# Optimization experiments

Hardware: AMD Instinct MI355X
Metric: run time of the kernel (lower is better)

Reference implementation:

```python
import jax, jax.numpy as jnp
import numpy as np

N = 100_000   # nodes
E = 1_600_000 # directed edges
G = 2048      # graphs in batch
NF = 78       # input node features
DIM = 32      # GIN hidden dim
L = 5         # num GIN layers
OUT = 128     # output_dim
BN_EPS = 1e-5


def setup_inputs() -> dict:
    key = jax.random.key(0)
    ks = jax.random.split(key, 8)
    s = 0.1
    return {
        "x": jax.random.normal(ks[0], (N, NF), jnp.float32),
        "edge_index": jax.random.randint(ks[1], (2, E), 0, N, jnp.int32),
        "batch": jnp.sort(jax.random.randint(ks[2], (N,), 0, G, jnp.int32)),
        "W1_0": (jax.random.normal(ks[3], (NF, DIM), jnp.float32) * s),
        "W1_rest": (jax.random.normal(ks[4], (L - 1, DIM, DIM), jnp.float32) * s),
        "b1": jnp.zeros((L, DIM), jnp.float32),
        "W2": (jax.random.normal(ks[5], (L, DIM, DIM), jnp.float32) * s),
        "b2": jnp.zeros((L, DIM), jnp.float32),
        "gamma": jnp.ones((L, DIM), jnp.float32),
        "beta": jnp.zeros((L, DIM), jnp.float32),
        "Wfc": (jax.random.normal(ks[6], (DIM, OUT), jnp.float32) * s),
        "bfc": jnp.zeros((OUT,), jnp.float32),
    }


def reference(x, edge_index, batch, W1_0, W1_rest, b1, W2, b2, gamma, beta, Wfc, bfc):
    src, dst = edge_index[0], edge_index[1]
    h = x
    for i in range(L):
        # GINConv (eps=0): h_i' = MLP(h_i + sum_{j->i} h_j)
        agg = jax.ops.segment_sum(h[src], dst, num_segments=N)  # [N, d]
        h = h + agg
        W1 = W1_0 if i == 0 else W1_rest[i - 1]
        h = jnp.maximum(h @ W1 + b1[i], 0.0) @ W2[i] + b2[i]
        # ReLU then BatchNorm1d (training mode: batch stats, biased var)
        h = jnp.maximum(h, 0.0)
        mu = h.mean(axis=0)
        var = h.var(axis=0)
        h = gamma[i] * (h - mu) * jax.lax.rsqrt(var + BN_EPS) + beta[i]
    pooled = jax.ops.segment_sum(h, batch, num_segments=G)  # global_add_pool [G, DIM]
    return jnp.maximum(pooled @ Wfc + bfc, 0.0)  # dropout is identity (eval)
```

## Files before the change

### kernel.cpp

```cpp
#include <hip/hip_runtime.h>
#include <hip/hip_fp16.h>

#define N_NODES 100000
#define N_EDGES 1600000
#define N_GRAPHS 2048
#define NFEAT 78
#define DIM 32
#define NLAYERS 5
#define OUTD 128
#define BN_EPS 1e-5f
#define NPB 32
#define NBUK 391
#define BNODES 256
#define STRIDE 4608
#define EPB 4096
#define NSLOTS2 ((N_NODES / NPB + 63) / 64)

__device__ __forceinline__ float2 up2(unsigned u) {
    __half2 h = *reinterpret_cast<__half2*>(&u);
    return __half22float2(h);
}
__device__ __forceinline__ unsigned pk2(float a, float b) {
    __half2 h = __floats2half2_rn(a, b);
    return *reinterpret_cast<unsigned*>(&h);
}

__global__ __launch_bounds__(256) void bfill2_kernel(
    const int* __restrict__ ei, int* __restrict__ bcnt, int* __restrict__ bdata)
{
    __shared__ int cur[NBUK];
    __shared__ int gbl[NBUK];
    int tid = threadIdx.x;
    int base = blockIdx.x * EPB;

    for (int i = tid; i < NBUK; i += 256) cur[i] = 0;
    __syncthreads();

    int ew[16];
    int eb[16];
    const int4* s4 = (const int4*)ei;
    const int4* d4 = (const int4*)(ei + N_EDGES);
#pragma unroll
    for (int c = 0; c < 4; ++c) {
        int eidx = base + c * 1024 + tid * 4;
        if (eidx < N_EDGES) {
            int4 sv = s4[eidx >> 2];
            int4 dv = d4[eidx >> 2];
            ew[c*4+0] = sv.x | ((dv.x & 255) << 17); eb[c*4+0] = dv.x >> 8;
            ew[c*4+1] = sv.y | ((dv.y & 255) << 17); eb[c*4+1] = dv.y >> 8;
            ew[c*4+2] = sv.z | ((dv.z & 255) << 17); eb[c*4+2] = dv.z >> 8;
            ew[c*4+3] = sv.w | ((dv.w & 255) << 17); eb[c*4+3] = dv.w >> 8;
        } else {
            eb[c*4+0] = eb[c*4+1] = eb[c*4+2] = eb[c*4+3] = -1;
            ew[c*4+0] = ew[c*4+1] = ew[c*4+2] = ew[c*4+3] = 0;
        }
    }

    int slot[16];
#pragma unroll
    for (int k = 0; k < 16; ++k)
        slot[k] = (eb[k] >= 0) ? atomicAdd(&cur[eb[k]], 1) : 0;
    __syncthreads();

    for (int b = tid; b < NBUK; b += 256) {
        int c = cur[b];
        gbl[b] = (c > 0) ? atomicAdd(&bcnt[b], c) : 0;
    }
    __syncthreads();

#pragma unroll
    for (int k = 0; k < 16; ++k) {
        int b = eb[k];
        if (b >= 0) {
            int pos = gbl[b] + slot[k];
            if (pos < STRIDE) bdata[b * STRIDE + pos] = ew[k];
        }
    }
}

__global__ __launch_bounds__(512) void bscan_kernel(
    const int* __restrict__ bcnt, int* __restrict__ bbase)
{
    __shared__ int sd[512];
    int t = threadIdx.x;
    int v = (t < NBUK) ? min(bcnt[t], STRIDE) : 0;
    sd[t] = v; __syncthreads();
    for (int off = 1; off < 512; off <<= 1) {
        int a = (t >= off) ? sd[t - off] : 0;
        __syncthreads();
        sd[t] += a;
        __syncthreads();
    }
    if (t < NBUK) bbase[t + 1] = sd[t];
    if (t == 0) bbase[0] = 0;
}

__global__ __launch_bounds__(256) void cfill2_kernel(
    const int* __restrict__ bcnt, const int* __restrict__ bbase,
    const int* __restrict__ bdata, int* __restrict__ edge_src,
    int* __restrict__ offs)
{
    __shared__ int sorted[STRIDE];
    __shared__ int cnt[BNODES], off[BNODES], cur[BNODES];
    int b = blockIdx.x, tid = threadIdx.x;
    int n = min(bcnt[b], STRIDE);
    int gb = bbase[b];
    const int* slab = bdata + (long)b * STRIDE;

    if (tid < BNODES) cnt[tid] = 0;
    __syncthreads();
    for (int i = tid; i < n; i += 256)
        atomicAdd(&cnt[slab[i] >> 17], 1);
    __syncthreads();
    int t = tid;
    if (t < BNODES) off[t] = cnt[t];
    __syncthreads();
    for (int o = 1; o < BNODES; o <<= 1) {
        int a = (t >= o && t < BNODES) ? off[t - o] : 0;
        __syncthreads();
        if (t < BNODES) off[t] += a;
        __syncthreads();
    }
    if (t < BNODES) {
        int excl = off[t] - cnt[t];
        off[t] = excl;
        cur[t] = excl;
        int node = b * BNODES + t;
        if (node <= N_NODES) offs[node] = gb + excl;
    }
    __syncthreads();
    for (int i = tid; i < n; i += 256) {
        int w = slab[i];
        int pos = atomicAdd(&cur[w >> 17], 1);
        sorted[pos] = w & 0x1FFFF;
    }
    __syncthreads();
    for (int i = tid; i < n; i += 256)
        edge_src[gb + i] = sorted[i];
}

__global__ __launch_bounds__(256) void gemm1_kernel(
    const float* __restrict__ h, const float* __restrict__ W,
    unsigned short* __restrict__ y)
{
    __shared__ float Wl[NFEAT * DIM];
    for (int i = threadIdx.x; i < NFEAT * DIM; i += 256) Wl[i] = W[i];
    __syncthreads();

    int t = blockIdx.x * 256 + threadIdx.x;
    int row = t >> 3;
    int c0 = (t & 7) * 4;

    float a0 = 0.f, a1 = 0.f, a2 = 0.f, a3 = 0.f;
    const float* hr = h + (long)row * NFEAT;
    for (int k = 0; k < NFEAT; ++k) {
        float xv = hr[k];
        a0 = fmaf(xv, Wl[k * DIM + c0 + 0], a0);
        a1 = fmaf(xv, Wl[k * DIM + c0 + 1], a1);
        a2 = fmaf(xv, Wl[k * DIM + c0 + 2], a2);
        a3 = fmaf(xv, Wl[k * DIM + c0 + 3], a3);
    }
    ((uint2*)y)[(long)row * 8 + (t & 7)] = make_uint2(pk2(a0, a1), pk2(a2, a3));
}

template<bool MM>
__global__ __launch_bounds__(256) void layer_kernel(
    const int* __restrict__ offs, const int* __restrict__ edge_src,
    const unsigned short* __restrict__ zin, const float* __restrict__ W1p,
    const float* __restrict__ cvec, const float* __restrict__ b1v,
    const float* __restrict__ W2, const float* __restrict__ b2v,
    unsigned short* __restrict__ zout, float* __restrict__ partial)
{
    __shared__ float W1l[DIM * DIM];
    __shared__ float W2l[DIM * DIM];
    __shared__ float zs[NPB][36];
    __shared__ float srow[NPB][36];
    __shared__ float b1l[DIM], b2l[DIM], cl[DIM];
    __shared__ float psum[DIM], psq[DIM];

    int tid = threadIdx.x;
    if (MM) for (int i = tid; i < DIM * DIM; i += 256) W1l[i] = W1p[i];
    for (int i = tid; i < DIM * DIM; i += 256) W2l[i] = W2[i];
    if (tid < DIM) {
        b1l[tid] = b1v[tid]; b2l[tid] = b2v[tid];
        cl[tid] = MM ? cvec[tid] : 0.f;
        psum[tid] = 0.f; psq[tid] = 0.f;
    }
    __syncthreads();

    int ln = tid >> 3, p = tid & 7;
    int c0 = p * 4;
    long node = (long)blockIdx.x * NPB + ln;
    int beg = offs[node], end = offs[node + 1];
    int deg = end - beg;
    const uint2* zb = (const uint2*)zin;

    uint2 sv = zb[node * 8 + p];
    float2 s01 = up2(sv.x), s23 = up2(sv.y);
    float a0 = s01.x, a1 = s01.y, a2 = s23.x, a3 = s23.y;
    int e = beg;
    for (; e + 8 <= end; e += 8) {
        uint2 v0 = zb[(long)edge_src[e + 0] * 8 + p];
        uint2 v1 = zb[(long)edge_src[e + 1] * 8 + p];
        uint2 v2 = zb[(long)edge_src[e + 2] * 8 + p];
        uint2 v3 = zb[(long)edge_src[e + 3] * 8 + p];
        uint2 v4 = zb[(long)edge_src[e + 4] * 8 + p];
        uint2 v5 = zb[(long)edge_src[e + 5] * 8 + p];
        uint2 v6 = zb[(long)edge_src[e + 6] * 8 + p];
        uint2 v7 = zb[(long)edge_src[e + 7] * 8 + p];
        float2 f;
        f = up2(v0.x); a0 += f.x; a1 += f.y;  f = up2(v0.y); a2 += f.x; a3 += f.y;
        f = up2(v1.x); a0 += f.x; a1 += f.y;  f = up2(v1.y); a2 += f.x; a3 += f.y;
        f = up2(v2.x); a0 += f.x; a1 += f.y;  f = up2(v2.y); a2 += f.x; a3 += f.y;
        f = up2(v3.x); a0 += f.x; a1 += f.y;  f = up2(v3.y); a2 += f.x; a3 += f.y;
        f = up2(v4.x); a0 += f.x; a1 += f.y;  f = up2(v4.y); a2 += f.x; a3 += f.y;
        f = up2(v5.x); a0 += f.x; a1 += f.y;  f = up2(v5.y); a2 += f.x; a3 += f.y;
        f = up2(v6.x); a0 += f.x; a1 += f.y;  f = up2(v6.y); a2 += f.x; a3 += f.y;
        f = up2(v7.x); a0 += f.x; a1 += f.y;  f = up2(v7.y); a2 += f.x; a3 += f.y;
    }
    for (; e < end; ++e) {
        uint2 v = zb[(long)edge_src[e] * 8 + p];
        float2 f;
        f = up2(v.x); a0 += f.x; a1 += f.y;
        f = up2(v.y); a2 += f.x; a3 += f.y;
    }
    *(float4*)&zs[ln][c0] = make_float4(a0, a1, a2, a3);
    __syncthreads();

    float sv4[4];
    if (MM) {
        sv4[0] = sv4[1] = sv4[2] = sv4[3] = 0.f;
#pragma unroll
        for (int k = 0; k < DIM; ++k) {
            float zk = zs[ln][k];
            sv4[0] = fmaf(zk, W1l[k * DIM + c0 + 0], sv4[0]);
            sv4[1] = fmaf(zk, W1l[k * DIM + c0 + 1], sv4[1]);
            sv4[2] = fmaf(zk, W1l[k * DIM + c0 + 2], sv4[2]);
            sv4[3] = fmaf(zk, W1l[k * DIM + c0 + 3], sv4[3]);
        }
        float dp1 = (float)(deg + 1);
#pragma unroll
        for (int j = 0; j < 4; ++j)
            sv4[j] = fmaf(dp1, cl[c0 + j], sv4[j]) + b1l[c0 + j];
    } else {
        sv4[0] = a0 + b1l[c0 + 0]; sv4[1] = a1 + b1l[c0 + 1];
        sv4[2] = a2 + b1l[c0 + 2]; sv4[3] = a3 + b1l[c0 + 3];
    }
    float4 srw = make_float4(fmaxf(sv4[0], 0.f), fmaxf(sv4[1], 0.f),
                             fmaxf(sv4[2], 0.f), fmaxf(sv4[3], 0.f));
    *(float4*)&srow[ln][c0] = srw;
    __syncthreads();

    float zv[4] = { b2l[c0 + 0], b2l[c0 + 1], b2l[c0 + 2], b2l[c0 + 3] };
#pragma unroll
    for (int k = 0; k < DIM; ++k) {
        float sk = srow[ln][k];
        zv[0] = fmaf(sk, W2l[k * DIM + c0 + 0], zv[0]);
        zv[1] = fmaf(sk, W2l[k * DIM + c0 + 1], zv[1]);
        zv[2] = fmaf(sk, W2l[k * DIM + c0 + 2], zv[2]);
        zv[3] = fmaf(sk, W2l[k * DIM + c0 + 3], zv[3]);
    }
#pragma unroll
    for (int j = 0; j < 4; ++j) zv[j] = fmaxf(zv[j], 0.f);
    ((uint2*)zout)[node * 8 + p] = make_uint2(pk2(zv[0], zv[1]), pk2(zv[2], zv[3]));

    float sq[4];
#pragma unroll
    for (int j = 0; j < 4; ++j) sq[j] = zv[j] * zv[j];
#pragma unroll
    for (int off = 8; off < 64; off <<= 1) {
#pragma unroll
        for (int j = 0; j < 4; ++j) {
            zv[j] += __shfl_xor(zv[j], off, 64);
            sq[j] += __shfl_xor(sq[j], off, 64);
        }
    }
    if ((tid & 63) < 8) {
#pragma unroll
        for (int j = 0; j < 4; ++j) {
            atomicAdd(&psum[c0 + j], zv[j]);
            atomicAdd(&psq[c0 + j], sq[j]);
        }
    }
    __syncthreads();
    if (tid < 2 * DIM) {
        float v = (tid < DIM) ? psum[tid] : psq[tid - DIM];
        atomicAdd(&partial[(long)(blockIdx.x >> 6) * 2 * DIM + tid], v);
    }
}

__global__ __launch_bounds__(256) void finalize_kernel(
    const float* __restrict__ partial,
    const float* __restrict__ gamma, const float* __restrict__ beta,
    float* __restrict__ ss, const float* W1next,
    float* __restrict__ W1p, float* __restrict__ cvec)
{
    __shared__ float red[256];
    __shared__ float sscl[DIM], sshl[DIM];
    int t = threadIdx.x;
    int c = t & 63;
    int chunk = t >> 6;
    float a = 0.f;
    for (int p = chunk; p < NSLOTS2; p += 4) a += partial[(long)p * 64 + c];
    red[t] = a; __syncthreads();
    if (t < 64) red[t] = red[t] + red[t + 64] + red[t + 128] + red[t + 192];
    __syncthreads();
    if (t < DIM) {
        const float invN = 1.0f / (float)N_NODES;
        float S = red[t], Q = red[t + DIM];
        float mu = S * invN;
        float var = Q * invN - mu * mu;
        float scale = gamma[t] * rsqrtf(var + BN_EPS);
        float shift = beta[t] - mu * scale;
        ss[t] = scale; ss[DIM + t] = shift;
        sscl[t] = scale; sshl[t] = shift;
    }
    __syncthreads();
    if (W1next) {
        for (int i = t; i < DIM * DIM; i += 256)
            W1p[i] = sscl[i >> 5] * W1next[i];
        if (t < DIM) {
            float cv = 0.f;
            for (int k = 0; k < DIM; ++k)
                cv += sshl[k] * W1next[k * DIM + t];
            cvec[t] = cv;
        }
    }
}

__global__ __launch_bounds__(256) void pool_kernel(
    const unsigned short* __restrict__ z, const int* __restrict__ batch,
    const float* __restrict__ ss, float* __restrict__ pooled)
{
    __shared__ float acc[32][32];
    __shared__ int slot[32];
    __shared__ int segg[32];
    __shared__ int nsegS;
    __shared__ float scl[DIM], shl[DIM];
    int tid = threadIdx.x;
    for (int i = tid; i < 1024; i += 256) ((float*)acc)[i] = 0.f;
    if (tid < DIM) { scl[tid] = ss[tid]; shl[tid] = ss[DIM + tid]; }
    int nodeBase = blockIdx.x * 32;
    if (tid < 32) {
        int nd = nodeBase + tid;
        int gv = batch[nd];
        int flag = (tid == 0) ? 1 : (gv != batch[nd - 1]);
        unsigned long long m = __ballot(flag);
        int s = __popcll(m & ((2ull << tid) - 1ull)) - 1;
        slot[tid] = s;
        if (flag) segg[s] = gv;
        if (tid == 0) nsegS = __popcll(m);
    }
    __syncthreads();

    int ln = tid >> 3;
    int p = tid & 7;
    long node = nodeBase + ln;
    uint2 u = ((const uint2*)z)[node * 8 + p];
    int c = p * 4;
    float2 f01 = up2(u.x), f23 = up2(u.y);
    float vx = fmaf(f01.x, scl[c+0], shl[c+0]);
    float vy = fmaf(f01.y, scl[c+1], shl[c+1]);
    float vz = fmaf(f23.x, scl[c+2], shl[c+2]);
    float vw = fmaf(f23.y, scl[c+3], shl[c+3]);
    int s = slot[ln];
    atomicAdd(&acc[s][c+0], vx);
    atomicAdd(&acc[s][c+1], vy);
    atomicAdd(&acc[s][c+2], vz);
    atomicAdd(&acc[s][c+3], vw);
    __syncthreads();

    int total = nsegS * 32;
    for (int i = tid; i < total; i += 256) {
        int r = i >> 5, dd = i & 31;
        float val = acc[r][dd];
        if (val != 0.f) atomicAdd(&pooled[(long)segg[r] * DIM + dd], val);
    }
}

__global__ __launch_bounds__(256) void fc_kernel(
    const float* __restrict__ pooled, const float* __restrict__ Wfc,
    const float* __restrict__ bfc, float* __restrict__ out)
{
    __shared__ float Wl[DIM * OUTD];
    for (int i = threadIdx.x; i < DIM * OUTD; i += 256) Wl[i] = Wfc[i];
    __syncthreads();
    int t = blockIdx.x * 256 + threadIdx.x;
    if (t >= N_GRAPHS * OUTD) return;
    int g = t >> 7;
    int o = t & (OUTD - 1);
    float acc = bfc[o];
    const float* pr = pooled + (long)g * DIM;
#pragma unroll
    for (int k = 0; k < DIM; ++k) acc += pr[k] * Wl[k * OUTD + o];
    out[t] = fmaxf(acc, 0.f);
}

extern "C" void kernel_launch(void* const* d_in, const int* in_sizes, int n_in,
                              void* d_out, int out_size, void* d_ws, size_t ws_size,
                              hipStream_t stream) {
    const float* x      = (const float*)d_in[0];
    const int*   ei     = (const int*)  d_in[1];
    const int*   batch  = (const int*)  d_in[2];
    const float* W1_0   = (const float*)d_in[3];
    const float* W1_rest= (const float*)d_in[4];
    const float* b1     = (const float*)d_in[5];
    const float* W2     = (const float*)d_in[6];
    const float* b2     = (const float*)d_in[7];
    const float* gamma  = (const float*)d_in[8];
    const float* beta   = (const float*)d_in[9];
    const float* Wfc    = (const float*)d_in[10];
    const float* bfc    = (const float*)d_in[11];
    float* out = (float*)d_out;

    int* wsi = (int*)d_ws;
    const size_t nf = (size_t)N_NODES * DIM;
    const size_t BD = (size_t)NBUK * STRIDE;
    int*   bdata  = wsi;
    unsigned short* zfpA = (unsigned short*)wsi;
    unsigned short* zfpB = (unsigned short*)(wsi + BD);
    int*   edge_src = wsi + BD + nf / 2;
    int*   offs   = edge_src + N_EDGES;
    int*   bcnt   = offs + (N_NODES + 1);
    int*   bbase  = bcnt + NBUK;
    float* pooled = (float*)(bbase + NBUK + 1);
    float* partial= pooled + (size_t)N_GRAPHS * DIM;
    float* ss     = partial + (size_t)NLAYERS * NSLOTS2 * 2 * DIM;
    float* W1p    = ss + NLAYERS * 2 * DIM;
    float* cvec   = W1p + NLAYERS * DIM * DIM;

    hipMemsetAsync(pooled, 0,
        ((size_t)N_GRAPHS * DIM + (size_t)NLAYERS * NSLOTS2 * 2 * DIM) *
        sizeof(float), stream);
    hipMemsetAsync(bcnt, 0, (size_t)NBUK * sizeof(int), stream);

    const int grpBlocks = (N_NODES * 8) / 256;
    const int NBLK = (N_EDGES + EPB - 1) / EPB;

    bfill2_kernel<<<NBLK, 256, 0, stream>>>(ei, bcnt, bdata);
    bscan_kernel<<<1, 512, 0, stream>>>(bcnt, bbase);
    cfill2_kernel<<<NBUK, 256, 0, stream>>>(bcnt, bbase, bdata, edge_src, offs);

    gemm1_kernel<<<grpBlocks, 256, 0, stream>>>(x, W1_0, zfpA);

    layer_kernel<false><<<N_NODES / NPB, 256, 0, stream>>>(
        offs, edge_src, zfpA, nullptr, nullptr,
        b1, W2, b2, zfpB, partial);
    finalize_kernel<<<1, 256, 0, stream>>>(
        partial, gamma, beta, ss,
        W1_rest, W1p + DIM * DIM, cvec + DIM);

    const unsigned short* zi = zfpB;
    unsigned short* zo = zfpA;
    for (int i = 1; i < NLAYERS; ++i) {
        layer_kernel<true><<<N_NODES / NPB, 256, 0, stream>>>(
            offs, edge_src, zi,
            W1p + (size_t)i * DIM * DIM, cvec + (size_t)i * DIM,
            b1 + i * DIM, W2 + (size_t)i * DIM * DIM, b2 + i * DIM,
            zo, partial + (size_t)i * NSLOTS2 * 2 * DIM);
        const float* W1next = (i + 1 < NLAYERS) ? (W1_rest + (size_t)i * DIM * DIM)
                                                : nullptr;
        finalize_kernel<<<1, 256, 0, stream>>>(
            partial + (size_t)i * NSLOTS2 * 2 * DIM,
            gamma + i * DIM, beta + i * DIM, ss + i * 2 * DIM,
            W1next, W1p + (size_t)(i + 1) * DIM * DIM,
            cvec + (size_t)(i + 1) * DIM);
        const unsigned short* tmp = zi; zi = zo; zo = (unsigned short*)tmp;
    }

    pool_kernel<<<N_NODES / 32, 256, 0, stream>>>(
        zi, batch, ss + (NLAYERS - 1) * 2 * DIM, pooled);
    fc_kernel<<<(N_GRAPHS * OUTD) / 256, 256, 0, stream>>>(pooled, Wfc, bfc, out);
}
```

Before: 311.1 us.

## Merge edge bucketing with first-layer GEMM and use shuffles in layer MLP

Edge bucket fill and the x@W1_0 projection now run as one kernel with a block-index split, removing a launch and letting the two independent jobs overlap. The workspace layout changes so the projected features no longer alias the bucket data, which that overlap requires. Inside the per-layer kernel, the two shared-memory staging arrays and their barriers are replaced by wavefront shuffles that pass the per-node row values between the 8 lanes owning a node. The shuffles add cross-lane instructions and selects, and the merged kernel uses more shared memory per block, which may reduce occupancy for the bucketing blocks.

```diff
diff --git a/kernel.cpp b/kernel.cpp
--- a/kernel.cpp
+++ b/kernel.cpp
@@ -14,6 +14,7 @@
 #define BNODES 256
 #define STRIDE 4608
 #define EPB 4096
+#define NBLK ((N_EDGES + EPB - 1) / EPB)
 #define NSLOTS2 ((N_NODES / NPB + 63) / 64)
 
 __device__ __forceinline__ float2 up2(unsigned u) {
@@ -25,56 +26,73 @@
     return *reinterpret_cast<unsigned*>(&h);
 }
 
-__global__ __launch_bounds__(256) void bfill2_kernel(
-    const int* __restrict__ ei, int* __restrict__ bcnt, int* __restrict__ bdata)
+__global__ __launch_bounds__(256) void prep_kernel(
+    const int* __restrict__ ei, int* __restrict__ bcnt, int* __restrict__ bdata,
+    const float* __restrict__ x, const float* __restrict__ W1_0,
+    unsigned short* __restrict__ y)
 {
     __shared__ int cur[NBUK];
     __shared__ int gbl[NBUK];
+    __shared__ float Wl[NFEAT * DIM];
     int tid = threadIdx.x;
-    int base = blockIdx.x * EPB;
-
-    for (int i = tid; i < NBUK; i += 256) cur[i] = 0;
-    __syncthreads();
-
-    int ew[16];
-    int eb[16];
-    const int4* s4 = (const int4*)ei;
-    const int4* d4 = (const int4*)(ei + N_EDGES);
-#pragma unroll
-    for (int c = 0; c < 4; ++c) {
-        int eidx = base + c * 1024 + tid * 4;
-        if (eidx < N_EDGES) {
-            int4 sv = s4[eidx >> 2];
-            int4 dv = d4[eidx >> 2];
-            ew[c*4+0] = sv.x | ((dv.x & 255) << 17); eb[c*4+0] = dv.x >> 8;
-            ew[c*4+1] = sv.y | ((dv.y & 255) << 17); eb[c*4+1] = dv.y >> 8;
-            ew[c*4+2] = sv.z | ((dv.z & 255) << 17); eb[c*4+2] = dv.z >> 8;
-            ew[c*4+3] = sv.w | ((dv.w & 255) << 17); eb[c*4+3] = dv.w >> 8;
-        } else {
-            eb[c*4+0] = eb[c*4+1] = eb[c*4+2] = eb[c*4+3] = -1;
-            ew[c*4+0] = ew[c*4+1] = ew[c*4+2] = ew[c*4+3] = 0;
-        }
-    }
-
-    int slot[16];
-#pragma unroll
-    for (int k = 0; k < 16; ++k)
-        slot[k] = (eb[k] >= 0) ? atomicAdd(&cur[eb[k]], 1) : 0;
-    __syncthreads();
-
-    for (int b = tid; b < NBUK; b += 256) {
-        int c = cur[b];
-        gbl[b] = (c > 0) ? atomicAdd(&bcnt[b], c) : 0;
-    }
-    __syncthreads();
-
-#pragma unroll
-    for (int k = 0; k < 16; ++k) {
-        int b = eb[k];
-        if (b >= 0) {
-            int pos = gbl[b] + slot[k];
-            if (pos < STRIDE) bdata[b * STRIDE + pos] = ew[k];
-        }
+
+    if (blockIdx.x < NBLK) {
+        int base = blockIdx.x * EPB;
+        for (int i = tid; i < NBUK; i += 256) cur[i] = 0;
+        __syncthreads();
+
+        int ew[16], eb[16];
+        const int4* s4 = (const int4*)ei;
+        const int4* d4 = (const int4*)(ei + N_EDGES);
+#pragma unroll
+        for (int c = 0; c < 4; ++c) {
+            int eidx = base + c * 1024 + tid * 4;
+            if (eidx < N_EDGES) {
+                int4 sv = s4[eidx >> 2];
+                int4 dv = d4[eidx >> 2];
+                ew[c*4+0] = sv.x | ((dv.x & 255) << 17); eb[c*4+0] = dv.x >> 8;
+                ew[c*4+1] = sv.y | ((dv.y & 255) << 17); eb[c*4+1] = dv.y >> 8;
+                ew[c*4+2] = sv.z | ((dv.z & 255) << 17); eb[c*4+2] = dv.z >> 8;
+                ew[c*4+3] = sv.w | ((dv.w & 255) << 17); eb[c*4+3] = dv.w >> 8;
+            } else {
+                eb[c*4+0] = eb[c*4+1] = eb[c*4+2] = eb[c*4+3] = -1;
+                ew[c*4+0] = ew[c*4+1] = ew[c*4+2] = ew[c*4+3] = 0;
+            }
+        }
+        int slot[16];
+#pragma unroll
+        for (int k = 0; k < 16; ++k)
+            slot[k] = (eb[k] >= 0) ? atomicAdd(&cur[eb[k]], 1) : 0;
+        __syncthreads();
+        for (int b = tid; b < NBUK; b += 256) {
+            int c = cur[b];
+            gbl[b] = (c > 0) ? atomicAdd(&bcnt[b], c) : 0;
+        }
+        __syncthreads();
+#pragma unroll
+        for (int k = 0; k < 16; ++k) {
+            int b = eb[k];
+            if (b >= 0) {
+                int pos = gbl[b] + slot[k];
+                if (pos < STRIDE) bdata[b * STRIDE + pos] = ew[k];
+            }
+        }
+    } else {
+        for (int i = tid; i < NFEAT * DIM; i += 256) Wl[i] = W1_0[i];
+        __syncthreads();
+        int t = (blockIdx.x - NBLK) * 256 + tid;
+        int row = t >> 3;
+        int c0 = (t & 7) * 4;
+        float a0 = 0.f, a1 = 0.f, a2 = 0.f, a3 = 0.f;
+        const float* hr = x + (long)row * NFEAT;
+        for (int k = 0; k < NFEAT; ++k) {
+            float xv = hr[k];
+            a0 = fmaf(xv, Wl[k * DIM + c0 + 0], a0);
+            a1 = fmaf(xv, Wl[k * DIM + c0 + 1], a1);
+            a2 = fmaf(xv, Wl[k * DIM + c0 + 2], a2);
+            a3 = fmaf(xv, Wl[k * DIM + c0 + 3], a3);
+        }
+        ((uint2*)y)[(long)row * 8 + (t & 7)] = make_uint2(pk2(a0, a1), pk2(a2, a3));
     }
 }
 
@@ -137,30 +155,6 @@
     __syncthreads();
     for (int i = tid; i < n; i += 256)
         edge_src[gb + i] = sorted[i];
-}
-
-__global__ __launch_bounds__(256) void gemm1_kernel(
-    const float* __restrict__ h, const float* __restrict__ W,
-    unsigned short* __restrict__ y)
-{
-    __shared__ float Wl[NFEAT * DIM];
-    for (int i = threadIdx.x; i < NFEAT * DIM; i += 256) Wl[i] = W[i];
-    __syncthreads();
-
-    int t = blockIdx.x * 256 + threadIdx.x;
-    int row = t >> 3;
-    int c0 = (t & 7) * 4;
-
-    float a0 = 0.f, a1 = 0.f, a2 = 0.f, a3 = 0.f;
-    const float* hr = h + (long)row * NFEAT;
-    for (int k = 0; k < NFEAT; ++k) {
-        float xv = hr[k];
-        a0 = fmaf(xv, Wl[k * DIM + c0 + 0], a0);
-        a1 = fmaf(xv, Wl[k * DIM + c0 + 1], a1);
-        a2 = fmaf(xv, Wl[k * DIM + c0 + 2], a2);
-        a3 = fmaf(xv, Wl[k * DIM + c0 + 3], a3);
-    }
-    ((uint2*)y)[(long)row * 8 + (t & 7)] = make_uint2(pk2(a0, a1), pk2(a2, a3));
 }
 
 template<bool MM>
@@ -173,8 +167,6 @@
 {
     __shared__ float W1l[DIM * DIM];
     __shared__ float W2l[DIM * DIM];
-    __shared__ float zs[NPB][36];
-    __shared__ float srow[NPB][36];
     __shared__ float b1l[DIM], b2l[DIM], cl[DIM];
     __shared__ float psum[DIM], psq[DIM];
 
@@ -190,14 +182,15 @@
 
     int ln = tid >> 3, p = tid & 7;
     int c0 = p * 4;
+    int gbase = (tid & 63) & ~7;
     long node = (long)blockIdx.x * NPB + ln;
     int beg = offs[node], end = offs[node + 1];
     int deg = end - beg;
     const uint2* zb = (const uint2*)zin;
 
     uint2 sv = zb[node * 8 + p];
-    float2 s01 = up2(sv.x), s23 = up2(sv.y);
-    float a0 = s01.x, a1 = s01.y, a2 = s23.x, a3 = s23.y;
+    float2 t01 = up2(sv.x), t23 = up2(sv.y);
+    float a0 = t01.x, a1 = t01.y, a2 = t23.x, a3 = t23.y;
     int e = beg;
     for (; e + 8 <= end; e += 8) {
         uint2 v0 = zb[(long)edge_src[e + 0] * 8 + p];
@@ -224,49 +217,49 @@
         f = up2(v.x); a0 += f.x; a1 += f.y;
         f = up2(v.y); a2 += f.x; a3 += f.y;
     }
-    *(float4*)&zs[ln][c0] = make_float4(a0, a1, a2, a3);
-    __syncthreads();
-
-    float sv4[4];
+
+    float r0, r1, r2, r3;
     if (MM) {
-        sv4[0] = sv4[1] = sv4[2] = sv4[3] = 0.f;
+        float s0 = 0.f, s1 = 0.f, s2 = 0.f, s3 = 0.f;
 #pragma unroll
         for (int k = 0; k < DIM; ++k) {
-            float zk = zs[ln][k];
-            sv4[0] = fmaf(zk, W1l[k * DIM + c0 + 0], sv4[0]);
-            sv4[1] = fmaf(zk, W1l[k * DIM + c0 + 1], sv4[1]);
-            sv4[2] = fmaf(zk, W1l[k * DIM + c0 + 2], sv4[2]);
-            sv4[3] = fmaf(zk, W1l[k * DIM + c0 + 3], sv4[3]);
+            float comp = ((k & 3) == 0) ? a0 : ((k & 3) == 1) ? a1
+                       : ((k & 3) == 2) ? a2 : a3;
+            float zk = __shfl(comp, gbase + (k >> 2), 64);
+            s0 = fmaf(zk, W1l[k * DIM + c0 + 0], s0);
+            s1 = fmaf(zk, W1l[k * DIM + c0 + 1], s1);
+            s2 = fmaf(zk, W1l[k * DIM + c0 + 2], s2);
+            s3 = fmaf(zk, W1l[k * DIM + c0 + 3], s3);
         }
         float dp1 = (float)(deg + 1);
-#pragma unroll
-        for (int j = 0; j < 4; ++j)
-            sv4[j] = fmaf(dp1, cl[c0 + j], sv4[j]) + b1l[c0 + j];
+        r0 = fmaxf(fmaf(dp1, cl[c0 + 0], s0) + b1l[c0 + 0], 0.f);
+        r1 = fmaxf(fmaf(dp1, cl[c0 + 1], s1) + b1l[c0 + 1], 0.f);
+        r2 = fmaxf(fmaf(dp1, cl[c0 + 2], s2) + b1l[c0 + 2], 0.f);
+        r3 = fmaxf(fmaf(dp1, cl[c0 + 3], s3) + b1l[c0 + 3], 0.f);
     } else {
-        sv4[0] = a0 + b1l[c0 + 0]; sv4[1] = a1 + b1l[c0 + 1];
-        sv4[2] = a2 + b1l[c0 + 2]; sv4[3] = a3 + b1l[c0 + 3];
-    }
-    float4 srw = make_float4(fmaxf(sv4[0], 0.f), fmaxf(sv4[1], 0.f),
-                             fmaxf(sv4[2], 0.f), fmaxf(sv4[3], 0.f));
-    *(float4*)&srow[ln][c0] = srw;
-    __syncthreads();
-
-    float zv[4] = { b2l[c0 + 0], b2l[c0 + 1], b2l[c0 + 2], b2l[c0 + 3] };
+        r0 = fmaxf(a0 + b1l[c0 + 0], 0.f);
+        r1 = fmaxf(a1 + b1l[c0 + 1], 0.f);
+        r2 = fmaxf(a2 + b1l[c0 + 2], 0.f);
+        r3 = fmaxf(a3 + b1l[c0 + 3], 0.f);
+    }
+
+    float z0 = b2l[c0 + 0], z1 = b2l[c0 + 1], z2 = b2l[c0 + 2], z3 = b2l[c0 + 3];
 #pragma unroll
     for (int k = 0; k < DIM; ++k) {
-        float sk = srow[ln][k];
-        zv[0] = fmaf(sk, W2l[k * DIM + c0 + 0], zv[0]);
-        zv[1] = fmaf(sk, W2l[k * DIM + c0 + 1], zv[1]);
-        zv[2] = fmaf(sk, W2l[k * DIM + c0 + 2], zv[2]);
-        zv[3] = fmaf(sk, W2l[k * DIM + c0 + 3], zv[3]);
-    }
-#pragma unroll
-    for (int j = 0; j < 4; ++j) zv[j] = fmaxf(zv[j], 0.f);
-    ((uint2*)zout)[node * 8 + p] = make_uint2(pk2(zv[0], zv[1]), pk2(zv[2], zv[3]));
-
-    float sq[4];
-#pragma unroll
-    for (int j = 0; j < 4; ++j) sq[j] = zv[j] * zv[j];
+        float comp = ((k & 3) == 0) ? r0 : ((k & 3) == 1) ? r1
+                   : ((k & 3) == 2) ? r2 : r3;
+        float rk = __shfl(comp, gbase + (k >> 2), 64);
+        z0 = fmaf(rk, W2l[k * DIM + c0 + 0], z0);
+        z1 = fmaf(rk, W2l[k * DIM + c0 + 1], z1);
+        z2 = fmaf(rk, W2l[k * DIM + c0 + 2], z2);
+        z3 = fmaf(rk, W2l[k * DIM + c0 + 3], z3);
+    }
+    z0 = fmaxf(z0, 0.f); z1 = fmaxf(z1, 0.f);
+    z2 = fmaxf(z2, 0.f); z3 = fmaxf(z3, 0.f);
+    ((uint2*)zout)[node * 8 + p] = make_uint2(pk2(z0, z1), pk2(z2, z3));
+
+    float zv[4] = { z0, z1, z2, z3 };
+    float sq[4] = { z0*z0, z1*z1, z2*z2, z3*z3 };
 #pragma unroll
     for (int off = 8; off < 64; off <<= 1) {
 #pragma unroll
@@ -417,9 +410,9 @@
     const size_t nf = (size_t)N_NODES * DIM;
     const size_t BD = (size_t)NBUK * STRIDE;
     int*   bdata  = wsi;
-    unsigned short* zfpA = (unsigned short*)wsi;
-    unsigned short* zfpB = (unsigned short*)(wsi + BD);
-    int*   edge_src = wsi + BD + nf / 2;
+    unsigned short* zfpA = (unsigned short*)(wsi + BD);
+    unsigned short* zfpB = zfpA + nf;
+    int*   edge_src = (int*)(zfpB + nf);
     int*   offs   = edge_src + N_EDGES;
     int*   bcnt   = offs + (N_NODES + 1);
     int*   bbase  = bcnt + NBUK;
@@ -435,13 +428,11 @@
     hipMemsetAsync(bcnt, 0, (size_t)NBUK * sizeof(int), stream);
 
     const int grpBlocks = (N_NODES * 8) / 256;
-    const int NBLK = (N_EDGES + EPB - 1) / EPB;
-
-    bfill2_kernel<<<NBLK, 256, 0, stream>>>(ei, bcnt, bdata);
+
+    prep_kernel<<<NBLK + grpBlocks, 256, 0, stream>>>(
+        ei, bcnt, bdata, x, W1_0, zfpA);
     bscan_kernel<<<1, 512, 0, stream>>>(bcnt, bbase);
     cfill2_kernel<<<NBUK, 256, 0, stream>>>(bcnt, bbase, bdata, edge_src, offs);
-
-    gemm1_kernel<<<grpBlocks, 256, 0, stream>>>(x, W1_0, zfpA);
 
     layer_kernel<false><<<N_NODES / NPB, 256, 0, stream>>>(
         offs, edge_src, zfpA, nullptr, nullptr,
```

Result: slower. 324.2 us (+4.2%).
